# Optimization experiments

Measured on AMD Instinct MI355X. Metric: run time of the kernel, lower is better.

The kernel has to match this reference:

```python
import jax, jax.numpy as jnp
import numpy as np

B, S, SC, E, H = 2, 2048, 2048, 1024, 16
D = E // H
EPS = 1e-6


def _layernorm(x, g, b):
    m = jnp.mean(x, axis=-1, keepdims=True)
    v = jnp.mean((x - m) ** 2, axis=-1, keepdims=True)
    return (x - m) / jnp.sqrt(v + EPS) * g + b


def _mha(xk, xv, xq, Wk, Wv, Wq, Wo, bo, masked):
    # per-head projections, vectorized over the head axis: [B,Sx,E] x [H,E,D] -> [B,H,Sx,D]
    K = jnp.einsum('bse,hed->bhsd', xk, Wk)
    V = jnp.einsum('bse,hed->bhsd', xv, Wv)
    Q = jnp.einsum('bqe,hed->bhqd', xq, Wq)
    scores = jnp.einsum('bhqd,bhkd->bhqk', Q, K)  # [B,H,Sq,Sk]
    sk = xk.shape[1]
    if masked:
        causal = jnp.triu(jnp.ones((xq.shape[1], sk), dtype=bool), k=1)
        scores = jnp.where(causal, -jnp.inf, scores)
    att = jax.nn.softmax(scores / jnp.sqrt(jnp.asarray(sk, scores.dtype)), axis=-1)
    out = jnp.einsum('bhqk,bhkd->bhqd', att, V)
    out = out.transpose(0, 2, 1, 3).reshape(out.shape[0], out.shape[2], -1)  # concat heads -> [B,Sq,E]
    return jax.nn.relu(out @ Wo + bo)  # Dense(emb_sz, relu) output projection


def setup_inputs():
    key = jax.random.key(0)
    ks = jax.random.split(key, 16)
    w = lambda k, shape: jax.random.normal(k, shape, jnp.float32) * 0.02
    return {
        'inputs': jax.random.normal(ks[0], (B, S, E), jnp.float32),
        'context_seq': jax.random.normal(ks[1], (B, SC, E), jnp.float32),
        'Wk1': w(ks[2], (H, E, D)), 'Wv1': w(ks[3], (H, E, D)), 'Wq1': w(ks[4], (H, E, D)),
        'Wo1': w(ks[5], (E, E)), 'bo1': jnp.zeros((E,), jnp.float32),
        'Wk2': w(ks[6], (H, E, D)), 'Wv2': w(ks[7], (H, E, D)), 'Wq2': w(ks[8], (H, E, D)),
        'Wo2': w(ks[9], (E, E)), 'bo2': jnp.zeros((E,), jnp.float32),
        'Wf': w(ks[10], (E, E)), 'bf': jnp.zeros((E,), jnp.float32),
        'g1': jnp.ones((E,), jnp.float32), 'b1': jnp.zeros((E,), jnp.float32),
        'g2': jnp.ones((E,), jnp.float32), 'b2': jnp.zeros((E,), jnp.float32),
        'g3': jnp.ones((E,), jnp.float32), 'b3': jnp.zeros((E,), jnp.float32),
    }


def reference(inputs, context_seq, Wk1, Wv1, Wq1, Wo1, bo1,
              Wk2, Wv2, Wq2, Wo2, bo2, Wf, bf,
              g1, b1, g2, b2, g3, b3):
    # masked multi-head self-attention + residual + LN1 (dropout is identity at inference)
    a = _mha(inputs, inputs, inputs, Wk1, Wv1, Wq1, Wo1, bo1, masked=True)
    a = _layernorm(inputs + a, g1, b1)
    # unmasked cross-attention: K/V from context, Q from previous output
    c = _mha(context_seq, context_seq, a, Wk2, Wv2, Wq2, Wo2, bo2, masked=False)
    c = _layernorm(c + c, g2, b2)  # faithful to source: residual adds output to itself
    # FFN (single Dense(emb_sz, relu)) + residual + LN3
    f = jax.nn.relu(c @ Wf + bf)
    return _layernorm(c + f, g3, b3)
```

## Files before the change

### kernel.cpp

```cpp
#include <hip/hip_runtime.h>
#include <stdint.h>
#include <stddef.h>

typedef __bf16 bf16;
typedef __bf16 bf16x8 __attribute__((ext_vector_type(8)));
typedef __bf16 bf16x4 __attribute__((ext_vector_type(4)));
typedef float  f32x4  __attribute__((ext_vector_type(4)));
typedef uint32_t u32x4 __attribute__((ext_vector_type(4)));

#define MFMA(a, b, c) __builtin_amdgcn_mfma_f32_16x16x32_bf16((a), (b), (c), 0, 0, 0)
#define SWZE(row, chunk) (((row) << 6) + ((((chunk) ^ ((row) & 7))) << 3))

static __device__ __forceinline__ void gload_lds16(const void* g, void* l) {
  __builtin_amdgcn_global_load_lds((const __attribute__((address_space(1))) void*)g,
                                   (__attribute__((address_space(3))) void*)l,
                                   16, 0, 0);
}
static __device__ __forceinline__ void waitvm0() {
  asm volatile("s_waitcnt vmcnt(0)" ::: "memory");
}
static __device__ __forceinline__ float expq(float x) {
  float r;
  asm("v_exp_f32 %0, %1" : "=v"(r) : "v"(x));
  return r;
}
static __device__ __forceinline__ float rcpq(float x) {
  float r;
  asm("v_rcp_f32 %0, %1" : "=v"(r) : "v"(x));
  return r;
}
static __device__ __forceinline__ uint32_t cvtpk_bf16(float lo, float hi) {
  uint32_t r;
  asm("v_cvt_pk_bf16_f32 %0, %1, %2" : "=v"(r) : "v"(lo), "v"(hi));
  return r;
}
static __device__ __forceinline__ int xcd_swz(int orig, int nwg) {
  return (orig & 7) * (nwg >> 3) + (orig >> 3);
}
static __device__ __forceinline__ int vperm_store(int s) {
  return (s & ~31) | (((s >> 3) & 1) << 4) | (((s >> 2) & 1) << 3) |
         (((s >> 4) & 1) << 2) | (s & 3);
}

__global__ __launch_bounds__(256) void prep_k(
    const float* __restrict__ inp, const float* __restrict__ ctx,
    bf16* __restrict__ XB, bf16* __restrict__ CB,
    const float* __restrict__ Wq1, const float* __restrict__ Wk1,
    const float* __restrict__ Wv1, const float* __restrict__ Wq2,
    const float* __restrict__ Wk2, const float* __restrict__ Wv2,
    bf16* __restrict__ WQKV1, bf16* __restrict__ WQ2, bf16* __restrict__ WKV2,
    const float* __restrict__ Wo1, const float* __restrict__ Wo2,
    const float* __restrict__ Wf,
    bf16* __restrict__ WO1, bf16* __restrict__ WO2, bf16* __restrict__ WFt) {
  const int tid = threadIdx.x;
  int bx = blockIdx.x;
  if (bx < 8192) {
    const float* s = bx < 4096 ? inp : ctx;
    bf16* d = bx < 4096 ? XB : CB;
    size_t idx = (size_t)(bx & 4095) * 256 + tid;
    float4 v = *(const float4*)(s + idx * 4);
    bf16x4 o;
    o[0] = (bf16)v.x; o[1] = (bf16)v.y; o[2] = (bf16)v.z; o[3] = (bf16)v.w;
    *(bf16x4*)(d + idx * 4) = o;
    return;
  }
  bx -= 8192;
  __shared__ float T[64][65];
  if (bx < 1536) {
    const int wi = bx >> 8, sub = bx & 255;
    const float* src = (wi == 0) ? Wq1 : (wi == 1) ? Wk1 : (wi == 2) ? Wv1
                     : (wi == 3) ? Wq2 : (wi == 4) ? Wk2 : Wv2;
    bf16* dst = (wi == 0) ? WQKV1 : (wi == 1) ? WQKV1 + 1048576
              : (wi == 2) ? WQKV1 + 2097152 : (wi == 3) ? WQ2
              : (wi == 4) ? WKV2 : WKV2 + 1048576;
    const int e0 = (sub & 15) * 64, h = sub >> 4;
    const int er = tid >> 4, dof = (tid & 15) * 4;
#pragma unroll
    for (int i = 0; i < 4; ++i) {
      int e = i * 16 + er;
      float4 v = *(const float4*)(src + ((size_t)h * 1024 + e0 + e) * 64 + dof);
      T[e][dof] = v.x; T[e][dof + 1] = v.y; T[e][dof + 2] = v.z; T[e][dof + 3] = v.w;
    }
    __syncthreads();
    const int dr = tid >> 3, eo = (tid & 7) * 8;
#pragma unroll
    for (int i = 0; i < 2; ++i) {
      int d = i * 32 + dr;
      bf16x8 ov;
#pragma unroll
      for (int j = 0; j < 8; ++j) ov[j] = (bf16)T[eo + j][d];
      *(bf16x8*)(dst + ((size_t)h * 64 + d) * 1024 + e0 + eo) = ov;
    }
    return;
  }
  bx -= 1536;
  {
    const int wi = bx >> 8, sub = bx & 255;
    const float* src = (wi == 0) ? Wo1 : (wi == 1) ? Wo2 : Wf;
    bf16* dst = (wi == 0) ? WO1 : (wi == 1) ? WO2 : WFt;
    const int k0 = (sub & 15) * 64, n0 = (sub >> 4) * 64;
    const int kr = tid >> 4, no = (tid & 15) * 4;
#pragma unroll
    for (int i = 0; i < 4; ++i) {
      int k = i * 16 + kr;
      float4 v = *(const float4*)(src + (size_t)(k0 + k) * 1024 + n0 + no);
      T[k][no] = v.x; T[k][no + 1] = v.y; T[k][no + 2] = v.z; T[k][no + 3] = v.w;
    }
    __syncthreads();
    const int nr = tid >> 3, ko = (tid & 7) * 8;
#pragma unroll
    for (int i = 0; i < 2; ++i) {
      int n = i * 32 + nr;
      bf16x8 ov;
#pragma unroll
      for (int j = 0; j < 8; ++j) ov[j] = (bf16)T[ko + j][n];
      *(bf16x8*)(dst + (size_t)(n0 + n) * 1024 + k0 + ko) = ov;
    }
  }
}

template <int EPI>
static __device__ __forceinline__ void gemm_body(
    const bf16* __restrict__ A, const bf16* __restrict__ Bt,
    bf16* __restrict__ Cb, float* __restrict__ Cf,
    const float* __restrict__ bias, const float* __restrict__ resid,
    int N, int K, float mul, int m0, int n0, bf16* As, bf16* Bs,
    bf16* __restrict__ Vt, int colV) {
  const int tid = threadIdx.x;
  const int l = tid & 63, w = tid >> 6;
  const int l15 = l & 15, g4 = l >> 4;
  const int wr = w >> 1, wc = w & 1;
  f32x4 acc[4][4] = {};
  const int crow = tid >> 3;
  const int cko = (tid & 7) * 8;
  for (int k0 = 0; k0 < K; k0 += 64) {
#pragma unroll
    for (int i = 0; i < 4; ++i) {
      int row = i * 32 + crow;
      gload_lds16(A + (size_t)(m0 + row) * K + (k0 + cko), (char*)As + (i * 256 + tid) * 16);
      gload_lds16(Bt + (size_t)(n0 + row) * K + (k0 + cko), (char*)Bs + (i * 256 + tid) * 16);
    }
    __syncthreads();
#pragma unroll
    for (int kk = 0; kk < 2; ++kk) {
      bf16x8 af[4], bfr[4];
#pragma unroll
      for (int x = 0; x < 4; ++x) {
        af[x]  = *(const bf16x8*)&As[(wr * 64 + x * 16 + l15) * 64 + kk * 32 + g4 * 8];
        bfr[x] = *(const bf16x8*)&Bs[(wc * 64 + x * 16 + l15) * 64 + kk * 32 + g4 * 8];
      }
      __builtin_amdgcn_s_setprio(1);
#pragma unroll
      for (int mf = 0; mf < 4; ++mf)
#pragma unroll
        for (int nf = 0; nf < 4; ++nf)
          acc[mf][nf] = MFMA(af[mf], bfr[nf], acc[mf][nf]);
      __builtin_amdgcn_s_setprio(0);
    }
    __syncthreads();
  }
  if (EPI == 2 && n0 >= colV) {
#pragma unroll
    for (int mf = 0; mf < 4; ++mf)
#pragma unroll
      for (int nf = 0; nf < 4; ++nf) {
        int colrel = n0 + wc * 64 + nf * 16 + l15 - colV;
        int h = colrel >> 6, d = colrel & 63;
        int row = m0 + wr * 64 + mf * 16 + g4 * 4;
        int b = row >> 11, s = row & 2047;
        bf16x4 pv;
#pragma unroll
        for (int r = 0; r < 4; ++r) pv[r] = (bf16)acc[mf][nf][r];
        *(bf16x4*)(Vt + (((size_t)(b * 16 + h) * 64 + d) * 2048 + vperm_store(s))) = pv;
      }
    return;
  }
#pragma unroll
  for (int mf = 0; mf < 4; ++mf)
#pragma unroll
    for (int nf = 0; nf < 4; ++nf)
#pragma unroll
      for (int r = 0; r < 4; ++r) {
        int row = m0 + wr * 64 + mf * 16 + g4 * 4 + r;
        int col = n0 + wc * 64 + nf * 16 + l15;
        size_t idx = (size_t)row * N + col;
        float v = acc[mf][nf][r];
        if (EPI == 1) {
          v = mul * fmaxf(v + bias[col], 0.f);
          if (resid) v += resid[idx];
          Cf[idx] = v;
        } else {
          Cb[idx] = (bf16)v;
        }
      }
}

__global__ __launch_bounds__(256) void gemm_qkv_k(
    const bf16* __restrict__ A, const bf16* __restrict__ Bt,
    bf16* __restrict__ Cb, bf16* __restrict__ Vt, int N, int K, int colV) {
  __shared__ __align__(16) bf16 As[128 * 64];
  __shared__ __align__(16) bf16 Bs[128 * 64];
  int swz = xcd_swz(blockIdx.y * gridDim.x + blockIdx.x, gridDim.x * gridDim.y);
  int bx = swz % gridDim.x, by = swz / gridDim.x;
  gemm_body<2>(A, Bt, Cb, nullptr, nullptr, nullptr, N, K, 1.f,
               by * 128, bx * 128, As, Bs, Vt, colV);
}

__global__ __launch_bounds__(256) void gemm_bt2_k(
    const bf16* __restrict__ A0, const bf16* __restrict__ Bt0, bf16* __restrict__ C0,
    const bf16* __restrict__ A1, const bf16* __restrict__ Bt1, bf16* __restrict__ C1,
    bf16* __restrict__ Vt, int K) {
  __shared__ __align__(16) bf16 As[128 * 64];
  __shared__ __align__(16) bf16 Bs[128 * 64];
  int swz = xcd_swz(blockIdx.y * gridDim.x + blockIdx.x, gridDim.x * gridDim.y);
  int bx = swz % gridDim.x, by = swz / gridDim.x;
  if (bx < 8)
    gemm_body<0>(A0, Bt0, C0, nullptr, nullptr, nullptr, 1024, K, 1.f,
                 by * 128, bx * 128, As, Bs, nullptr, 1 << 30);
  else
    gemm_body<2>(A1, Bt1, C1, nullptr, nullptr, nullptr, 2048, K, 1.f,
                 by * 128, (bx - 8) * 128, As, Bs, Vt, 1024);
}

template <int EPI>
__global__ __launch_bounds__(512) void gemm64_k(
    const bf16* __restrict__ A, const bf16* __restrict__ Bt,
    bf16* __restrict__ Cb, float* __restrict__ Cf,
    const float* __restrict__ bias, const float* __restrict__ resid,
    int N, int K, float mul) {
  __shared__ __align__(16) bf16 As[64 * 64];
  __shared__ __align__(16) bf16 Bs[128 * 64];
  const int tid = threadIdx.x;
  const int l = tid & 63, w = tid >> 6;
  const int l15 = l & 15, g4 = l >> 4;
  const int wr = w >> 2, wc = w & 3;
  int swz = xcd_swz(blockIdx.y * gridDim.x + blockIdx.x, gridDim.x * gridDim.y);
  const int m0 = (swz / gridDim.x) * 64, n0 = (swz % gridDim.x) * 128;
  f32x4 acc[2][2] = {};
  const int crow = tid >> 3, cko = (tid & 7) * 8;
  for (int k0 = 0; k0 < K; k0 += 64) {
    gload_lds16(A + (size_t)(m0 + crow) * K + (k0 + cko), (char*)As + tid * 16);
#pragma unroll
    for (int i = 0; i < 2; ++i) {
      int row = i * 64 + crow;
      gload_lds16(Bt + (size_t)(n0 + row) * K + (k0 + cko), (char*)Bs + (i * 512 + tid) * 16);
    }
    __syncthreads();
#pragma unroll
    for (int kk = 0; kk < 2; ++kk) {
      bf16x8 af[2], bfr[2];
#pragma unroll
      for (int x = 0; x < 2; ++x) {
        af[x]  = *(const bf16x8*)&As[(wr * 32 + x * 16 + l15) * 64 + kk * 32 + g4 * 8];
        bfr[x] = *(const bf16x8*)&Bs[(wc * 32 + x * 16 + l15) * 64 + kk * 32 + g4 * 8];
      }
      __builtin_amdgcn_s_setprio(1);
#pragma unroll
      for (int mf = 0; mf < 2; ++mf)
#pragma unroll
        for (int nf = 0; nf < 2; ++nf)
          acc[mf][nf] = MFMA(af[mf], bfr[nf], acc[mf][nf]);
      __builtin_amdgcn_s_setprio(0);
    }
    __syncthreads();
  }
#pragma unroll
  for (int mf = 0; mf < 2; ++mf)
#pragma unroll
    for (int nf = 0; nf < 2; ++nf)
#pragma unroll
      for (int r = 0; r < 4; ++r) {
        int row = m0 + wr * 32 + mf * 16 + g4 * 4 + r;
        int col = n0 + wc * 32 + nf * 16 + l15;
        size_t idx = (size_t)row * N + col;
        float v = acc[mf][nf][r];
        if (EPI == 0) {
          Cb[idx] = (bf16)v;
        } else {
          v = mul * fmaxf(v + bias[col], 0.f);
          if (resid) v += resid[idx];
          Cf[idx] = v;
        }
      }
}

template <int CAUSAL>
__global__ __launch_bounds__(256) void attn_k(
    const bf16* __restrict__ Q, int ldq, size_t sBq,
    const bf16* __restrict__ Kp, int ldk, size_t sBk,
    const bf16* __restrict__ Vt,
    bf16* __restrict__ O, int ldo, size_t sBo,
    int Sk) {
  __shared__ __align__(16) bf16 Ks[2][64 * 64];
  __shared__ __align__(16) bf16 Vs[2][64 * 64];
  const int tid = threadIdx.x;
  const int l = tid & 63, w = tid >> 6;
  const int l15 = l & 15, g4 = l >> 4;
  const int orig = blockIdx.y * gridDim.x + blockIdx.x;
  int qt, bh;
  if (CAUSAL) {
    const int slot = orig >> 8, s = orig & 255;
    const int pb = s & 31;
    qt = (slot & 1) ? (31 - pb) : pb;
    bh = (s >> 5) * 4 + slot;
  } else {
    const int swz = xcd_swz(orig, gridDim.x * gridDim.y);
    qt = swz % gridDim.x;
    bh = swz / gridDim.x;
  }
  const int b = bh >> 4, h = bh & 15;
  const int nT = Sk >> 6;
  const int total = CAUSAL ? (qt + 1) : nT;
  const int q0w = qt * 64 + w * 16;
  const bf16* Qb = Q + (size_t)b * sBq + h * 64;
  const bf16* Kb = Kp + (size_t)b * sBk + h * 64;
  const bf16* Vb = Vt + ((size_t)bh * 64) * Sk;
  bf16* Ob = O + (size_t)b * sBo + h * 64;
  const float sc2 = rsqrtf((float)Sk) * 1.442695040888963f;

  bf16x8 qf[2];
#pragma unroll
  for (int kk = 0; kk < 2; ++kk) {
    bf16x8 t8 = *(const bf16x8*)(Qb + (size_t)(q0w + l15) * ldq + kk * 32 + g4 * 8);
#pragma unroll
    for (int j = 0; j < 8; ++j) t8[j] = (bf16)((float)t8[j] * sc2);
    qf[kk] = t8;
  }

  bf16x8 onesb;
#pragma unroll
  for (int j = 0; j < 8; ++j) onesb[j] = (bf16)1.0f;

  f32x4 o[4] = {};
  f32x4 ol = {};

  const int srow = tid >> 3, sj = tid & 7;
  auto stage = [&](int ch, int bufi) {
#pragma unroll
    for (int ii = 0; ii < 2; ++ii) {
      int row = ii * 32 + srow;
      int je = ((sj ^ (row & 7)) << 3);
      gload_lds16(Kb + (size_t)(ch * 64 + row) * ldk + je,
                  (char*)&Ks[bufi][0] + (ii * 256 + tid) * 16);
      gload_lds16(Vb + (size_t)row * Sk + ch * 64 + je,
                  (char*)&Vs[bufi][0] + (ii * 256 + tid) * 16);
    }
  };

  stage(0, 0);
  waitvm0();
  __builtin_amdgcn_s_barrier();

  int cur = 0;

  for (int i = 0; i < total; ++i) {
    if (i + 1 < total) stage(i + 1, cur ^ 1);

    const int k0 = i * 64;
    const bf16* ks = Ks[cur];
    const bf16* vs = Vs[cur];

    f32x4 s[4] = {};
    __builtin_amdgcn_s_setprio(1);
#pragma unroll
    for (int nf = 0; nf < 4; ++nf)
#pragma unroll
      for (int kk = 0; kk < 2; ++kk) {
        bf16x8 kf = *(const bf16x8*)&ks[SWZE(nf * 16 + l15, kk * 4 + g4)];
        s[nf] = MFMA(kf, qf[kk], s[nf]);
      }
    __builtin_amdgcn_s_setprio(0);

    if (CAUSAL && i == total - 1) {
#pragma unroll
      for (int nf = 0; nf < 4; ++nf)
#pragma unroll
        for (int r = 0; r < 4; ++r)
          if ((k0 + nf * 16 + g4 * 4 + r) > (q0w + l15)) s[nf][r] = -3e38f;
    }

#pragma unroll
    for (int nf = 0; nf < 4; ++nf) {
      s[nf][0] = expq(s[nf][0]);
      s[nf][1] = expq(s[nf][1]);
      s[nf][2] = expq(s[nf][2]);
      s[nf][3] = expq(s[nf][3]);
    }

    __builtin_amdgcn_s_setprio(1);
#pragma unroll
    for (int kk = 0; kk < 2; ++kk) {
      u32x4 td;
      td[0] = cvtpk_bf16(s[2 * kk][0],     s[2 * kk][1]);
      td[1] = cvtpk_bf16(s[2 * kk][2],     s[2 * kk][3]);
      td[2] = cvtpk_bf16(s[2 * kk + 1][0], s[2 * kk + 1][1]);
      td[3] = cvtpk_bf16(s[2 * kk + 1][2], s[2 * kk + 1][3]);
      bf16x8 pa = __builtin_bit_cast(bf16x8, td);
#pragma unroll
      for (int nf2 = 0; nf2 < 4; ++nf2) {
        bf16x8 vf = *(const bf16x8*)&vs[SWZE(nf2 * 16 + l15, kk * 4 + g4)];
        o[nf2] = MFMA(pa, vf, o[nf2]);
      }
      ol = MFMA(pa, onesb, ol);
    }
    __builtin_amdgcn_s_setprio(0);

    waitvm0();
    __builtin_amdgcn_s_barrier();
    cur ^= 1;
  }

  {
    float inv[4];
#pragma unroll
    for (int r = 0; r < 4; ++r) inv[r] = rcpq(ol[r]);
#pragma unroll
    for (int nf2 = 0; nf2 < 4; ++nf2)
#pragma unroll
      for (int r = 0; r < 4; ++r)
        Ob[(size_t)(q0w + g4 * 4 + r) * ldo + nf2 * 16 + l15] = (bf16)(o[nf2][r] * inv[r]);
  }
}

__global__ __launch_bounds__(256) void ln_k(const float* __restrict__ X,
                                            const float* __restrict__ g,
                                            const float* __restrict__ bta,
                                            bf16* __restrict__ outb,
                                            float* __restrict__ outf) {
  const int tid = threadIdx.x;
  const size_t row = blockIdx.x;
  const float* x = X + row * 1024;
  float4 v = *(const float4*)(x + tid * 4);
  float sum = v.x + v.y + v.z + v.w;
  float sq = v.x * v.x + v.y * v.y + v.z * v.z + v.w * v.w;
#pragma unroll
  for (int m = 1; m < 64; m <<= 1) {
    sum += __shfl_xor(sum, m);
    sq += __shfl_xor(sq, m);
  }
  __shared__ float s1[4], s2[4];
  int w = tid >> 6;
  if ((tid & 63) == 0) { s1[w] = sum; s2[w] = sq; }
  __syncthreads();
  sum = s1[0] + s1[1] + s1[2] + s1[3];
  sq = s2[0] + s2[1] + s2[2] + s2[3];
  float mean = sum * (1.f / 1024.f);
  float var = sq * (1.f / 1024.f) - mean * mean;
  float inv = rsqrtf(var + 1e-6f);
  float4 gv = *(const float4*)(g + tid * 4);
  float4 bv = *(const float4*)(bta + tid * 4);
  float y0 = (v.x - mean) * inv * gv.x + bv.x;
  float y1 = (v.y - mean) * inv * gv.y + bv.y;
  float y2 = (v.z - mean) * inv * gv.z + bv.z;
  float y3 = (v.w - mean) * inv * gv.w + bv.w;
  if (outb) {
    bf16x4 ob;
    ob[0] = (bf16)y0; ob[1] = (bf16)y1; ob[2] = (bf16)y2; ob[3] = (bf16)y3;
    *(bf16x4*)(outb + row * 1024 + tid * 4) = ob;
  }
  if (outf) {
    float4 of;
    of.x = y0; of.y = y1; of.z = y2; of.w = y3;
    *(float4*)(outf + row * 1024 + tid * 4) = of;
  }
}

extern "C" void kernel_launch(void* const* d_in, const int* in_sizes, int n_in,
                              void* d_out, int out_size, void* d_ws, size_t ws_size,
                              hipStream_t stream) {
  (void)in_sizes; (void)n_in; (void)out_size; (void)ws_size;
  const float* inp = (const float*)d_in[0];
  const float* ctx = (const float*)d_in[1];
  const float* Wk1 = (const float*)d_in[2];
  const float* Wv1 = (const float*)d_in[3];
  const float* Wq1 = (const float*)d_in[4];
  const float* Wo1 = (const float*)d_in[5];
  const float* bo1 = (const float*)d_in[6];
  const float* Wk2 = (const float*)d_in[7];
  const float* Wv2 = (const float*)d_in[8];
  const float* Wq2 = (const float*)d_in[9];
  const float* Wo2 = (const float*)d_in[10];
  const float* bo2 = (const float*)d_in[11];
  const float* Wf = (const float*)d_in[12];
  const float* bfp = (const float*)d_in[13];
  const float* g1 = (const float*)d_in[14];
  const float* b1 = (const float*)d_in[15];
  const float* g2 = (const float*)d_in[16];
  const float* b2 = (const float*)d_in[17];
  const float* g3 = (const float*)d_in[18];
  const float* b3 = (const float*)d_in[19];
  float* out = (float*)d_out;

  char* ws = (char*)d_ws;
  size_t off = 0;
  auto alloc = [&](size_t bytes) {
    char* p = ws + off;
    off += (bytes + 255) & ~(size_t)255;
    return p;
  };
  bf16* XB = (bf16*)alloc(4096ULL * 1024 * 2);
  bf16* CB = (bf16*)alloc(4096ULL * 1024 * 2);
  bf16* WQKV1 = (bf16*)alloc(3072ULL * 1024 * 2);
  bf16* WO1 = (bf16*)alloc(1024ULL * 1024 * 2);
  bf16* WQ2 = (bf16*)alloc(1024ULL * 1024 * 2);
  bf16* WKV2 = (bf16*)alloc(2048ULL * 1024 * 2);
  bf16* WO2 = (bf16*)alloc(1024ULL * 1024 * 2);
  bf16* WFt = (bf16*)alloc(1024ULL * 1024 * 2);
  bf16* QKV1 = (bf16*)alloc(4096ULL * 3072 * 2);
  bf16* V1T = (bf16*)alloc(32ULL * 64 * 2048 * 2);
  bf16* ATT1 = (bf16*)alloc(4096ULL * 1024 * 2);
  float* T1 = (float*)alloc(4096ULL * 1024 * 4);
  float* CF = (float*)alloc(4096ULL * 1024 * 4);

  bf16* AB = XB;
  bf16* CBf = CB;
  bf16* Q2 = QKV1;
  bf16* KV2 = QKV1 + 4096ULL * 1024;
  bf16* V2T = V1T;
  bf16* ATT2 = ATT1;
  float* T2 = T1;
  float* T3 = T1;

  dim3 b256(256);
  dim3 b512(512);

  prep_k<<<10496, b256, 0, stream>>>(inp, ctx, XB, CB,
                                     Wq1, Wk1, Wv1, Wq2, Wk2, Wv2,
                                     WQKV1, WQ2, WKV2,
                                     Wo1, Wo2, Wf, WO1, WO2, WFt);

  gemm_qkv_k<<<dim3(24, 32), b256, 0, stream>>>(XB, WQKV1, QKV1, V1T, 3072, 1024, 2048);
  attn_k<1><<<dim3(32, 32), b256, 0, stream>>>(QKV1, 3072, (size_t)2048 * 3072,
                                               QKV1 + 1024, 3072, (size_t)2048 * 3072,
                                               V1T, ATT1, 1024, (size_t)2048 * 1024, 2048);
  gemm64_k<1><<<dim3(8, 64), b512, 0, stream>>>(ATT1, WO1, nullptr, T1, bo1, inp,
                                                1024, 1024, 1.f);
  ln_k<<<4096, b256, 0, stream>>>(T1, g1, b1, AB, nullptr);

  gemm_bt2_k<<<dim3(24, 32), b256, 0, stream>>>(AB, WQ2, Q2, CB, WKV2, KV2, V2T, 1024);
  attn_k<0><<<dim3(32, 32), b256, 0, stream>>>(Q2, 1024, (size_t)2048 * 1024,
                                               KV2, 2048, (size_t)2048 * 2048,
                                               V2T, ATT2, 1024, (size_t)2048 * 1024, 2048);
  gemm64_k<1><<<dim3(8, 64), b512, 0, stream>>>(ATT2, WO2, nullptr, T2, bo2, nullptr,
                                                1024, 1024, 2.f);
  ln_k<<<4096, b256, 0, stream>>>(T2, g2, b2, CBf, CF);

  gemm64_k<1><<<dim3(8, 64), b512, 0, stream>>>(CBf, WFt, nullptr, T3, bfp, CF,
                                                1024, 1024, 1.f);
  ln_k<<<4096, b256, 0, stream>>>(T3, g3, b3, nullptr, out);
}
```

Before: 265.8 us.

## Triple-buffer K and split K/V staging with partial vmcnt waits in attention

Rewrites the attention kernel's load pipeline. K tiles are now triple-buffered and prefetched two iterations ahead, and V tiles are staged separately mid-iteration. A partial vmcnt(4) wait plus an extra barrier between the QK and PV phases replaces the full drain at the end of each iteration. The aim is to hide global-to-LDS latency behind compute, at the cost of more LDS, a second barrier per iteration and redundant clamped loads on the tail iterations.

```diff
diff --git a/kernel.cpp b/kernel.cpp
--- a/kernel.cpp
+++ b/kernel.cpp
@@ -18,6 +18,9 @@
 }
 static __device__ __forceinline__ void waitvm0() {
   asm volatile("s_waitcnt vmcnt(0)" ::: "memory");
+}
+static __device__ __forceinline__ void waitvm4() {
+  asm volatile("s_waitcnt vmcnt(4)" ::: "memory");
 }
 static __device__ __forceinline__ float expq(float x) {
   float r;
@@ -291,7 +294,7 @@
     const bf16* __restrict__ Vt,
     bf16* __restrict__ O, int ldo, size_t sBo,
     int Sk) {
-  __shared__ __align__(16) bf16 Ks[2][64 * 64];
+  __shared__ __align__(16) bf16 Ks[3][64 * 64];
   __shared__ __align__(16) bf16 Vs[2][64 * 64];
   const int tid = threadIdx.x;
   const int l = tid & 63, w = tid >> 6;
@@ -335,30 +338,40 @@
   f32x4 ol = {};
 
   const int srow = tid >> 3, sj = tid & 7;
-  auto stage = [&](int ch, int bufi) {
+  auto stageK = [&](int ch, int bufi) {
 #pragma unroll
     for (int ii = 0; ii < 2; ++ii) {
       int row = ii * 32 + srow;
       int je = ((sj ^ (row & 7)) << 3);
       gload_lds16(Kb + (size_t)(ch * 64 + row) * ldk + je,
                   (char*)&Ks[bufi][0] + (ii * 256 + tid) * 16);
+    }
+  };
+  auto stageV = [&](int ch, int bufi) {
+#pragma unroll
+    for (int ii = 0; ii < 2; ++ii) {
+      int row = ii * 32 + srow;
+      int je = ((sj ^ (row & 7)) << 3);
       gload_lds16(Vb + (size_t)row * Sk + ch * 64 + je,
                   (char*)&Vs[bufi][0] + (ii * 256 + tid) * 16);
     }
   };
 
-  stage(0, 0);
-  waitvm0();
+  stageK(0, 0);
+  stageK(total > 1 ? 1 : 0, 1);
+  stageV(0, 0);
+  waitvm4();
   __builtin_amdgcn_s_barrier();
 
-  int cur = 0;
+  int kc = 0, vc = 0;
 
   for (int i = 0; i < total; ++i) {
-    if (i + 1 < total) stage(i + 1, cur ^ 1);
+    const int kst = (kc + 2 >= 3) ? (kc - 1) : (kc + 2);
+    stageK(i + 2 < total ? i + 2 : total - 1, kst);
 
     const int k0 = i * 64;
-    const bf16* ks = Ks[cur];
-    const bf16* vs = Vs[cur];
+    const bf16* ks = Ks[kc];
+    const bf16* vs = Vs[vc];
 
     f32x4 s[4] = {};
     __builtin_amdgcn_s_setprio(1);
@@ -387,15 +400,25 @@
       s[nf][3] = expq(s[nf][3]);
     }
 
+    u32x4 td0, td1;
+    td0[0] = cvtpk_bf16(s[0][0], s[0][1]);
+    td0[1] = cvtpk_bf16(s[0][2], s[0][3]);
+    td0[2] = cvtpk_bf16(s[1][0], s[1][1]);
+    td0[3] = cvtpk_bf16(s[1][2], s[1][3]);
+    td1[0] = cvtpk_bf16(s[2][0], s[2][1]);
+    td1[1] = cvtpk_bf16(s[2][2], s[2][3]);
+    td1[2] = cvtpk_bf16(s[3][0], s[3][1]);
+    td1[3] = cvtpk_bf16(s[3][2], s[3][3]);
+
+    stageV(i + 1 < total ? i + 1 : total - 1, vc ^ 1);
+
+    waitvm4();
+    __builtin_amdgcn_s_barrier();
+
     __builtin_amdgcn_s_setprio(1);
 #pragma unroll
     for (int kk = 0; kk < 2; ++kk) {
-      u32x4 td;
-      td[0] = cvtpk_bf16(s[2 * kk][0],     s[2 * kk][1]);
-      td[1] = cvtpk_bf16(s[2 * kk][2],     s[2 * kk][3]);
-      td[2] = cvtpk_bf16(s[2 * kk + 1][0], s[2 * kk + 1][1]);
-      td[3] = cvtpk_bf16(s[2 * kk + 1][2], s[2 * kk + 1][3]);
-      bf16x8 pa = __builtin_bit_cast(bf16x8, td);
+      bf16x8 pa = __builtin_bit_cast(bf16x8, kk == 0 ? td0 : td1);
 #pragma unroll
       for (int nf2 = 0; nf2 < 4; ++nf2) {
         bf16x8 vf = *(const bf16x8*)&vs[SWZE(nf2 * 16 + l15, kk * 4 + g4)];
@@ -405,9 +428,9 @@
     }
     __builtin_amdgcn_s_setprio(0);
 
-    waitvm0();
     __builtin_amdgcn_s_barrier();
-    cur ^= 1;
+    kc = (kc == 2) ? 0 : kc + 1;
+    vc ^= 1;
   }
 
   {
```

Measured after the change: 270.5 us. No clear change (+1.8%).

## Split attention warps 2x2 over query and key halves with LDS reduction

Applied to the files above, without the earlier changes.

Each of the four warps in the attention kernel now covers 32 query rows and half of each 64-key tile, where before each warp took 16 query rows over the whole tile. Every K and V fragment read from LDS now feeds two MFMAs instead of one, which cuts LDS read traffic per MFMA. The two key-half partial outputs and row sums are combined at the end through shared memory, with kh==1 warps writing and kh==0 warps finishing the normalisation and store. This adds register pressure, an extra barrier and LDS traffic in the epilogue, and half the warps sit idle during the final store.

```diff
diff --git a/kernel.cpp b/kernel.cpp
--- a/kernel.cpp
+++ b/kernel.cpp
@@ -291,11 +291,13 @@
     const bf16* __restrict__ Vt,
     bf16* __restrict__ O, int ldo, size_t sBo,
     int Sk) {
-  __shared__ __align__(16) bf16 Ks[2][64 * 64];
-  __shared__ __align__(16) bf16 Vs[2][64 * 64];
+  __shared__ __align__(16) char smem[32768];
+  bf16* const KsBase = (bf16*)smem;
+  bf16* const VsBase = (bf16*)(smem + 16384);
   const int tid = threadIdx.x;
   const int l = tid & 63, w = tid >> 6;
   const int l15 = l & 15, g4 = l >> 4;
+  const int qh = w >> 1, kh = w & 1;
   const int orig = blockIdx.y * gridDim.x + blockIdx.x;
   int qt, bh;
   if (CAUSAL) {
@@ -311,28 +313,31 @@
   const int b = bh >> 4, h = bh & 15;
   const int nT = Sk >> 6;
   const int total = CAUSAL ? (qt + 1) : nT;
-  const int q0w = qt * 64 + w * 16;
+  const int q0b = qt * 64;
   const bf16* Qb = Q + (size_t)b * sBq + h * 64;
   const bf16* Kb = Kp + (size_t)b * sBk + h * 64;
   const bf16* Vb = Vt + ((size_t)bh * 64) * Sk;
   bf16* Ob = O + (size_t)b * sBo + h * 64;
   const float sc2 = rsqrtf((float)Sk) * 1.442695040888963f;
 
-  bf16x8 qf[2];
-#pragma unroll
-  for (int kk = 0; kk < 2; ++kk) {
-    bf16x8 t8 = *(const bf16x8*)(Qb + (size_t)(q0w + l15) * ldq + kk * 32 + g4 * 8);
-#pragma unroll
-    for (int j = 0; j < 8; ++j) t8[j] = (bf16)((float)t8[j] * sc2);
-    qf[kk] = t8;
-  }
+  bf16x8 qf[2][2];
+#pragma unroll
+  for (int qg = 0; qg < 2; ++qg)
+#pragma unroll
+    for (int kk = 0; kk < 2; ++kk) {
+      bf16x8 t8 = *(const bf16x8*)(Qb + (size_t)(q0b + qh * 32 + qg * 16 + l15) * ldq +
+                                   kk * 32 + g4 * 8);
+#pragma unroll
+      for (int j = 0; j < 8; ++j) t8[j] = (bf16)((float)t8[j] * sc2);
+      qf[qg][kk] = t8;
+    }
 
   bf16x8 onesb;
 #pragma unroll
   for (int j = 0; j < 8; ++j) onesb[j] = (bf16)1.0f;
 
-  f32x4 o[4] = {};
-  f32x4 ol = {};
+  f32x4 o[2][4] = {};
+  f32x4 ol[2] = {};
 
   const int srow = tid >> 3, sj = tid & 7;
   auto stage = [&](int ch, int bufi) {
@@ -341,9 +346,9 @@
       int row = ii * 32 + srow;
       int je = ((sj ^ (row & 7)) << 3);
       gload_lds16(Kb + (size_t)(ch * 64 + row) * ldk + je,
-                  (char*)&Ks[bufi][0] + (ii * 256 + tid) * 16);
+                  (char*)(KsBase + bufi * 4096) + (ii * 256 + tid) * 16);
       gload_lds16(Vb + (size_t)row * Sk + ch * 64 + je,
-                  (char*)&Vs[bufi][0] + (ii * 256 + tid) * 16);
+                  (char*)(VsBase + bufi * 4096) + (ii * 256 + tid) * 16);
     }
   };
 
@@ -357,51 +362,60 @@
     if (i + 1 < total) stage(i + 1, cur ^ 1);
 
     const int k0 = i * 64;
-    const bf16* ks = Ks[cur];
-    const bf16* vs = Vs[cur];
-
-    f32x4 s[4] = {};
+    const bf16* ks = KsBase + cur * 4096;
+    const bf16* vs = VsBase + cur * 4096;
+
+    f32x4 s[2][2] = {};
     __builtin_amdgcn_s_setprio(1);
 #pragma unroll
-    for (int nf = 0; nf < 4; ++nf)
+    for (int ksub = 0; ksub < 2; ++ksub)
 #pragma unroll
       for (int kk = 0; kk < 2; ++kk) {
-        bf16x8 kf = *(const bf16x8*)&ks[SWZE(nf * 16 + l15, kk * 4 + g4)];
-        s[nf] = MFMA(kf, qf[kk], s[nf]);
+        bf16x8 kf = *(const bf16x8*)&ks[SWZE(kh * 32 + ksub * 16 + l15, kk * 4 + g4)];
+        s[ksub][0] = MFMA(kf, qf[0][kk], s[ksub][0]);
+        s[ksub][1] = MFMA(kf, qf[1][kk], s[ksub][1]);
       }
     __builtin_amdgcn_s_setprio(0);
 
     if (CAUSAL && i == total - 1) {
 #pragma unroll
-      for (int nf = 0; nf < 4; ++nf)
-#pragma unroll
-        for (int r = 0; r < 4; ++r)
-          if ((k0 + nf * 16 + g4 * 4 + r) > (q0w + l15)) s[nf][r] = -3e38f;
-    }
-
-#pragma unroll
-    for (int nf = 0; nf < 4; ++nf) {
-      s[nf][0] = expq(s[nf][0]);
-      s[nf][1] = expq(s[nf][1]);
-      s[nf][2] = expq(s[nf][2]);
-      s[nf][3] = expq(s[nf][3]);
-    }
+      for (int ksub = 0; ksub < 2; ++ksub)
+#pragma unroll
+        for (int qg = 0; qg < 2; ++qg)
+#pragma unroll
+          for (int r = 0; r < 4; ++r)
+            if ((k0 + kh * 32 + ksub * 16 + g4 * 4 + r) > (q0b + qh * 32 + qg * 16 + l15))
+              s[ksub][qg][r] = -3e38f;
+    }
+
+#pragma unroll
+    for (int ksub = 0; ksub < 2; ++ksub)
+#pragma unroll
+      for (int qg = 0; qg < 2; ++qg) {
+        s[ksub][qg][0] = expq(s[ksub][qg][0]);
+        s[ksub][qg][1] = expq(s[ksub][qg][1]);
+        s[ksub][qg][2] = expq(s[ksub][qg][2]);
+        s[ksub][qg][3] = expq(s[ksub][qg][3]);
+      }
+
+    bf16x8 vf[4];
+#pragma unroll
+    for (int nf2 = 0; nf2 < 4; ++nf2)
+      vf[nf2] = *(const bf16x8*)&vs[SWZE(nf2 * 16 + l15, kh * 4 + g4)];
 
     __builtin_amdgcn_s_setprio(1);
 #pragma unroll
-    for (int kk = 0; kk < 2; ++kk) {
+    for (int qg = 0; qg < 2; ++qg) {
       u32x4 td;
-      td[0] = cvtpk_bf16(s[2 * kk][0],     s[2 * kk][1]);
-      td[1] = cvtpk_bf16(s[2 * kk][2],     s[2 * kk][3]);
-      td[2] = cvtpk_bf16(s[2 * kk + 1][0], s[2 * kk + 1][1]);
-      td[3] = cvtpk_bf16(s[2 * kk + 1][2], s[2 * kk + 1][3]);
+      td[0] = cvtpk_bf16(s[0][qg][0], s[0][qg][1]);
+      td[1] = cvtpk_bf16(s[0][qg][2], s[0][qg][3]);
+      td[2] = cvtpk_bf16(s[1][qg][0], s[1][qg][1]);
+      td[3] = cvtpk_bf16(s[1][qg][2], s[1][qg][3]);
       bf16x8 pa = __builtin_bit_cast(bf16x8, td);
 #pragma unroll
-      for (int nf2 = 0; nf2 < 4; ++nf2) {
-        bf16x8 vf = *(const bf16x8*)&vs[SWZE(nf2 * 16 + l15, kk * 4 + g4)];
-        o[nf2] = MFMA(pa, vf, o[nf2]);
-      }
-      ol = MFMA(pa, onesb, ol);
+      for (int nf2 = 0; nf2 < 4; ++nf2)
+        o[qg][nf2] = MFMA(pa, vf[nf2], o[qg][nf2]);
+      ol[qg] = MFMA(pa, onesb, ol[qg]);
     }
     __builtin_amdgcn_s_setprio(0);
 
@@ -411,14 +425,38 @@
   }
 
   {
-    float inv[4];
-#pragma unroll
-    for (int r = 0; r < 4; ++r) inv[r] = rcpq(ol[r]);
-#pragma unroll
-    for (int nf2 = 0; nf2 < 4; ++nf2)
-#pragma unroll
-      for (int r = 0; r < 4; ++r)
-        Ob[(size_t)(q0w + g4 * 4 + r) * ldo + nf2 * 16 + l15] = (bf16)(o[nf2][r] * inv[r]);
+    float* sc = (float*)smem;
+    float* my = sc + (size_t)(qh * 64 + l) * 41;
+    if (kh == 1) {
+#pragma unroll
+      for (int qg = 0; qg < 2; ++qg) {
+#pragma unroll
+        for (int nf2 = 0; nf2 < 4; ++nf2)
+#pragma unroll
+          for (int r = 0; r < 4; ++r) my[(qg * 4 + nf2) * 4 + r] = o[qg][nf2][r];
+#pragma unroll
+        for (int r = 0; r < 4; ++r) my[32 + qg * 4 + r] = ol[qg][r];
+      }
+    }
+    __syncthreads();
+    if (kh == 0) {
+#pragma unroll
+      for (int qg = 0; qg < 2; ++qg) {
+        f32x4 lsum;
+#pragma unroll
+        for (int r = 0; r < 4; ++r) lsum[r] = ol[qg][r] + my[32 + qg * 4 + r];
+        float inv[4];
+#pragma unroll
+        for (int r = 0; r < 4; ++r) inv[r] = rcpq(lsum[r]);
+#pragma unroll
+        for (int nf2 = 0; nf2 < 4; ++nf2)
+#pragma unroll
+          for (int r = 0; r < 4; ++r) {
+            float v = (o[qg][nf2][r] + my[(qg * 4 + nf2) * 4 + r]) * inv[r];
+            Ob[(size_t)(q0b + qh * 32 + qg * 16 + g4 * 4 + r) * ldo + nf2 * 16 + l15] = (bf16)v;
+          }
+      }
+    }
   }
 }
 
```

Result: no change. 264.4 us (-0.5%).
